# Performance work log

Hardware: AMD Instinct MI355X
Metric: run time of the kernel (lower is better)

Reference implementation:

```python
import jax, jax.numpy as jnp
import numpy as np

N_NODES = 100000
N_EDGES = 1600000
IN_CH = 64
HID = 64
OUT_CH = 16


def setup_inputs() -> dict:
    key = jax.random.key(0)
    ks = jax.random.split(key, 8)
    x = jax.random.normal(ks[0], (N_NODES, IN_CH), dtype=jnp.float32)
    edge_index = jax.random.randint(ks[1], (2, N_EDGES), 0, N_NODES, dtype=jnp.int64)
    s = 1.0 / np.sqrt(IN_CH)
    W1l = jax.random.normal(ks[2], (HID, IN_CH), dtype=jnp.float32) * s
    W1r = jax.random.normal(ks[3], (HID, IN_CH), dtype=jnp.float32) * s
    b1 = jnp.zeros((HID,), dtype=jnp.float32)
    W2l = jax.random.normal(ks[4], (HID, HID), dtype=jnp.float32) * s
    W2r = jax.random.normal(ks[5], (HID, HID), dtype=jnp.float32) * s
    b2 = jnp.zeros((HID,), dtype=jnp.float32)
    Wlin = jax.random.normal(ks[6], (OUT_CH, HID), dtype=jnp.float32) * s
    blin = jnp.zeros((OUT_CH,), dtype=jnp.float32)
    return {"x": x, "edge_index": edge_index, "W1l": W1l, "b1": b1, "W1r": W1r,
            "W2l": W2l, "b2": b2, "W2r": W2r, "Wlin": Wlin, "blin": blin}


def _sage_conv(x, src, dst, Wl, b, Wr):
    # PyG SAGEConv with mean aggregation:
    # out = lin_l(mean_{j in N(i)} x_j) + lin_r(x_i); bias lives in lin_l.
    msgs = x[src]                                              # [E, F] gather
    summed = jax.ops.segment_sum(msgs, dst, num_segments=N_NODES)  # [N, F]
    cnt = jax.ops.segment_sum(jnp.ones((src.shape[0],), x.dtype), dst,
                              num_segments=N_NODES)            # [N]
    agg = summed / jnp.maximum(cnt, 1.0)[:, None]              # mean, deg-0 safe
    return agg @ Wl.T + b + x @ Wr.T


def reference(x, edge_index, W1l, b1, W1r, W2l, b2, W2r, Wlin, blin):
    src, dst = edge_index[0], edge_index[1]
    h = jax.nn.relu(_sage_conv(x, src, dst, W1l, b1, W1r))
    h = jax.nn.relu(_sage_conv(h, src, dst, W2l, b2, W2r))
    return h @ Wlin.T + blin
```

## Files before the change

kernel.cpp:

```cpp
#include <hip/hip_runtime.h>

#define NN 100000
#define NE 1600000

#define BSHIFT 9
#define BWIDTH 512
#define NBUCK 196
#define SLOTS 12288
#define CHUNK 2048
#define B1_BLOCKS ((NE + CHUNK - 1) / CHUNK)
#define GEMM_BLOCKS ((NN + 63) / 64)

typedef float    v2f __attribute__((ext_vector_type(2)));
typedef unsigned v2u __attribute__((ext_vector_type(2)));
typedef short    bf16x8 __attribute__((ext_vector_type(8)));
typedef float    f32x4  __attribute__((ext_vector_type(4)));

__device__ __forceinline__ float u2f(unsigned u) {
    union { unsigned u; float f; } v; v.u = u; return v.f;
}
__device__ __forceinline__ unsigned f2u(float f) {
    union { float f; unsigned u; } v; v.f = f; return v.u;
}
__device__ __forceinline__ unsigned f2bf(float f) {
    unsigned u = f2u(f);
    return (u + 0x7FFFu + ((u >> 16) & 1u)) >> 16;
}
__device__ __forceinline__ v2f unpk(unsigned x) {
    v2u w; w[0] = x << 16; w[1] = x & 0xFFFF0000u;
    union { v2u u; v2f f; } c; c.u = w; return c.f;
}

__global__ void detect_mode_kernel(const int* ei32, int* flag, int* bcnt) {
    __shared__ int any_nonzero;
    if (threadIdx.x == 0) any_nonzero = 0;
    if (threadIdx.x < NBUCK) bcnt[threadIdx.x] = 0;
    __syncthreads();
    int idx = 1 + 2 * threadIdx.x;
    if (ei32[idx] != 0) atomicOr(&any_nonzero, 1);
    __syncthreads();
    if (threadIdx.x == 0) flag[0] = (any_nonzero == 0) ? 1 : 0;
}

__device__ __forceinline__ void load_edge(const void* ei, int is64, int e,
                                          int& s, int& d) {
    if (is64) {
        const long long* p = (const long long*)ei;
        s = (int)p[e];
        d = (int)p[NE + e];
    } else {
        const int* p = (const int*)ei;
        s = p[e];
        d = p[NE + e];
    }
}

template<int BF16IN>
__device__ __forceinline__ void gemm_mfma_body(
    char* smem, const void* __restrict__ featv,
    const float* __restrict__ Wl, const float* __restrict__ Wr,
    const float* __restrict__ bias,
    unsigned* __restrict__ outt, unsigned* __restrict__ outr,
    int tile, int t)
{
    unsigned short* Als = (unsigned short*)smem;
    unsigned short* Bls = (unsigned short*)(smem + 9216);
    const int lane = t & 63, w = t >> 6;
    const int m0 = tile * 64;
    const float*    featf = (const float*)featv;
    const unsigned* featu = (const unsigned*)featv;

    #pragma unroll
    for (int rep = 0; rep < 2; ++rep) {
        int task = t + 256 * rep;
        int row = task >> 3, s = task & 7;
        int gn = m0 + row;
        uint4 u;
        if (BF16IN) {
            u = (gn < NN) ? *(const uint4*)(featu + (size_t)gn * 32 + 4 * s)
                          : make_uint4(0u, 0u, 0u, 0u);
        } else {
            if (gn < NN) {
                float4 v0 = *(const float4*)(featf + (size_t)gn * 64 + 8 * s);
                float4 v1 = *(const float4*)(featf + (size_t)gn * 64 + 8 * s + 4);
                u.x = f2bf(v0.x) | (f2bf(v0.y) << 16);
                u.y = f2bf(v0.z) | (f2bf(v0.w) << 16);
                u.z = f2bf(v1.x) | (f2bf(v1.y) << 16);
                u.w = f2bf(v1.z) | (f2bf(v1.w) << 16);
            } else u = make_uint4(0u, 0u, 0u, 0u);
        }
        *(uint4*)(Als + row * 72 + 8 * s) = u;
    }
    #pragma unroll
    for (int rep = 0; rep < 4; ++rep) {
        int task = t + 256 * rep;
        int c = task >> 3, s = task & 7;
        const float* Wsrc = (c < 64) ? (Wl + (size_t)c * 64)
                                     : (Wr + (size_t)(c - 64) * 64);
        float4 v0 = *(const float4*)(Wsrc + 8 * s);
        float4 v1 = *(const float4*)(Wsrc + 8 * s + 4);
        uint4 u;
        u.x = f2bf(v0.x) | (f2bf(v0.y) << 16);
        u.y = f2bf(v0.z) | (f2bf(v0.w) << 16);
        u.z = f2bf(v1.x) | (f2bf(v1.y) << 16);
        u.w = f2bf(v1.z) | (f2bf(v1.w) << 16);
        *(uint4*)(Bls + c * 72 + 8 * s) = u;
    }
    __syncthreads();

    const int r = lane & 15, g = lane >> 4;
    const int cw0 = 32 * w;

    bf16x8 bf[2][2];
    #pragma unroll
    for (int ct = 0; ct < 2; ++ct)
        #pragma unroll
        for (int ks = 0; ks < 2; ++ks) {
            int c = cw0 + 16 * ct + r;
            bf[ct][ks] = *(const bf16x8*)(Bls + c * 72 + (ks * 4 + g) * 8);
        }

    f32x4 acc[4][2];
    #pragma unroll
    for (int nt = 0; nt < 4; ++nt)
        #pragma unroll
        for (int ct = 0; ct < 2; ++ct)
            acc[nt][ct] = (f32x4){0.f, 0.f, 0.f, 0.f};

    #pragma unroll
    for (int nt = 0; nt < 4; ++nt) {
        bf16x8 af[2];
        #pragma unroll
        for (int ks = 0; ks < 2; ++ks) {
            int rr = nt * 16 + r;
            af[ks] = *(const bf16x8*)(Als + rr * 72 + (ks * 4 + g) * 8);
        }
        #pragma unroll
        for (int ct = 0; ct < 2; ++ct)
            #pragma unroll
            for (int ks = 0; ks < 2; ++ks)
                acc[nt][ct] = __builtin_amdgcn_mfma_f32_16x16x32_bf16(
                    af[ks], bf[ct][ks], acc[nt][ct], 0, 0, 0);
    }

    unsigned short* Tb = (unsigned short*)outt;
    unsigned short* Rb = (unsigned short*)outr;
    #pragma unroll
    for (int ct = 0; ct < 2; ++ct) {
        int c = cw0 + 16 * ct + r;
        float badd = (c >= 64) ? bias[c - 64] : 0.f;
        unsigned short* dst = (c < 64) ? (Tb + c) : (Rb + (c - 64));
        #pragma unroll
        for (int nt = 0; nt < 4; ++nt)
            #pragma unroll
            for (int i = 0; i < 4; ++i) {
                int row = m0 + nt * 16 + g * 4 + i;
                if (row < NN)
                    dst[(size_t)row * 64] = (unsigned short)f2bf(acc[nt][ct][i] + badd);
            }
    }
}

__global__ __launch_bounds__(256) void b1_gemm1_kernel(
    const void* ei, const int* flag,
    int* __restrict__ bcnt, int2* __restrict__ bpairs,
    const float* __restrict__ x,
    const float* __restrict__ W1l, const float* __restrict__ W1r,
    const float* __restrict__ b1,
    unsigned* __restrict__ T, unsigned* __restrict__ R)
{
    __shared__ __align__(16) char smem[27648];
    const int t = threadIdx.x;

    if (blockIdx.x >= B1_BLOCKS) {
        if (blockIdx.x == B1_BLOCKS && t < 32) T[(size_t)NN * 32 + t] = 0u;
        gemm_mfma_body<0>(smem, x, W1l, W1r, b1, T, R, blockIdx.x - B1_BLOCKS, t);
        return;
    }

    int2* stage = (int2*)smem;
    unsigned short* sbuck = (unsigned short*)(smem + 16384);
    int* hist  = (int*)(smem + 20480);
    int* scanb = (int*)(smem + 21264);
    int* gbase = (int*)(smem + 22048);
    int* lofs  = (int*)(smem + 22832);
    int* sc    = (int*)(smem + 23616);

    const int is64 = *flag;
    const int e0 = blockIdx.x * CHUNK;
    const int nE = min(CHUNK, NE - e0);

    for (int i = t; i < NBUCK; i += 256) { hist[i] = 0; lofs[i] = 0; }
    __syncthreads();

    int sr[8], dr[8];
    #pragma unroll
    for (int rr = 0; rr < 8; ++rr) {
        int e = e0 + t + 256 * rr;
        if (e < NE) load_edge(ei, is64, e, sr[rr], dr[rr]);
        else dr[rr] = -1;
    }
    #pragma unroll
    for (int rr = 0; rr < 8; ++rr)
        if (dr[rr] >= 0) atomicAdd(&hist[dr[rr] >> BSHIFT], 1);
    __syncthreads();

    int v = (t < NBUCK) ? hist[t] : 0;
    sc[t] = v;
    __syncthreads();
    for (int off = 1; off < 256; off <<= 1) {
        int u = (t >= off) ? sc[t - off] : 0;
        __syncthreads();
        sc[t] += u;
        __syncthreads();
    }
    if (t < NBUCK) {
        scanb[t] = sc[t] - v;
        gbase[t] = atomicAdd(&bcnt[t], v);
    }
    __syncthreads();

    #pragma unroll
    for (int rr = 0; rr < 8; ++rr) {
        if (dr[rr] >= 0) {
            int b = dr[rr] >> BSHIFT;
            int p = scanb[b] + atomicAdd(&lofs[b], 1);
            stage[p] = make_int2(sr[rr], dr[rr]);
            sbuck[p] = (unsigned short)b;
        }
    }
    __syncthreads();

    for (int i = t; i < nE; i += 256) {
        int b = sbuck[i];
        int off = gbase[b] + (i - scanb[b]);
        if (off < SLOTS) bpairs[(size_t)b * SLOTS + off] = stage[i];
    }
}

__global__ __launch_bounds__(512) void bucket_to_csr_kernel(
    const int* __restrict__ bcnt, const int2* __restrict__ bpairs,
    int* __restrict__ rowptr, int* __restrict__ colb)
{
    __shared__ int ldeg[512], lptr[512], lcnt[512], sc[512];
    const int t = threadIdx.x, b = blockIdx.x;

    int v = (t < NBUCK) ? bcnt[t] : 0;
    sc[t] = v;
    __syncthreads();
    for (int off = 1; off < 512; off <<= 1) {
        int u = (t >= off) ? sc[t - off] : 0;
        __syncthreads();
        sc[t] += u;
        __syncthreads();
    }
    const int base = (b == 0) ? 0 : sc[b - 1];
    if (b == 0 && t == 0) rowptr[NN] = NE;
    __syncthreads();

    ldeg[t] = 0; lcnt[t] = 0;
    __syncthreads();

    const int n0 = b << BSHIFT;
    const int cnt = min(bcnt[b], SLOTS);
    const int2* src = bpairs + (size_t)b * SLOTS;
    for (int i = t; i < cnt; i += 512)
        atomicAdd(&ldeg[src[i].y - n0], 1);
    __syncthreads();

    int a = ldeg[t];
    sc[t] = a;
    __syncthreads();
    for (int off = 1; off < 512; off <<= 1) {
        int u = (t >= off) ? sc[t - off] : 0;
        __syncthreads();
        sc[t] += u;
        __syncthreads();
    }
    lptr[t] = sc[t] - a;
    __syncthreads();

    int gn = n0 + t;
    if (gn < NN) rowptr[gn] = base + lptr[t];

    for (int i = t; i < cnt; i += 512) {
        int2 p = src[i];
        int li = p.y - n0;
        int pos = lptr[li] + atomicAdd(&lcnt[li], 1);
        colb[base + pos] = p.x << 7;
    }
}

__global__ __launch_bounds__(256) void gemm2_kernel(
    const unsigned* __restrict__ feat,
    const float* __restrict__ Wl, const float* __restrict__ Wr,
    const float* __restrict__ bias,
    unsigned* __restrict__ outt, unsigned* __restrict__ outr)
{
    __shared__ __align__(16) char smem[27648];
    gemm_mfma_body<1>(smem, feat, Wl, Wr, bias, outt, outr, blockIdx.x, threadIdx.x);
}

__global__ void aggregate_relu_kernel(const int* __restrict__ rowptr,
                                      const int* __restrict__ colb,
                                      const unsigned* __restrict__ tt,
                                      unsigned* rh) {
    const int wv   = (blockIdx.x * blockDim.x + threadIdx.x) >> 6;
    const int lane = threadIdx.x & 63;
    const int half = lane >> 5;
    const int slot = (lane >> 3) & 3;
    const int c8   = lane & 7;
    const int node = 2 * wv + half;
    if (node >= NN) return;

    const int beg = rowptr[node], end = rowptr[node + 1];
    const int deg = end - beg;
    int niter = (deg + 3) >> 2;
    niter = max(niter, __shfl_xor(niter, 32));

    const char* tb = (const char*)tt;
    const int zoff = NN * 128;
    v2f a0 = {0.f, 0.f}, a1 = {0.f, 0.f}, a2 = {0.f, 0.f}, a3 = {0.f, 0.f};
    v2f b0 = {0.f, 0.f}, b1 = {0.f, 0.f}, b2 = {0.f, 0.f}, b3 = {0.f, 0.f};

    int jj = beg + slot;
    int it = 0;
    for (; it + 4 <= niter; it += 4, jj += 16) {
        int jc0 = min(jj,      end - 1);
        int jc1 = min(jj + 4,  end - 1);
        int jc2 = min(jj + 8,  end - 1);
        int jc3 = min(jj + 12, end - 1);
        int o0 = colb[jc0];
        int o1 = colb[jc1];
        int o2 = colb[jc2];
        int o3 = colb[jc3];
        o0 = (jj      < end) ? o0 : zoff;
        o1 = (jj + 4  < end) ? o1 : zoff;
        o2 = (jj + 8  < end) ? o2 : zoff;
        o3 = (jj + 12 < end) ? o3 : zoff;
        uint4 u0 = *(const uint4*)(tb + (size_t)(unsigned)o0 + 16 * c8);
        uint4 u1 = *(const uint4*)(tb + (size_t)(unsigned)o1 + 16 * c8);
        uint4 u2 = *(const uint4*)(tb + (size_t)(unsigned)o2 + 16 * c8);
        uint4 u3 = *(const uint4*)(tb + (size_t)(unsigned)o3 + 16 * c8);
        a0 += unpk(u0.x); a1 += unpk(u0.y); a2 += unpk(u0.z); a3 += unpk(u0.w);
        b0 += unpk(u1.x); b1 += unpk(u1.y); b2 += unpk(u1.z); b3 += unpk(u1.w);
        a0 += unpk(u2.x); a1 += unpk(u2.y); a2 += unpk(u2.z); a3 += unpk(u2.w);
        b0 += unpk(u3.x); b1 += unpk(u3.y); b2 += unpk(u3.z); b3 += unpk(u3.w);
    }
    for (; it < niter; ++it, jj += 4) {
        int jc0 = min(jj, end - 1);
        int o0 = colb[jc0];
        o0 = (jj < end) ? o0 : zoff;
        uint4 u0 = *(const uint4*)(tb + (size_t)(unsigned)o0 + 16 * c8);
        a0 += unpk(u0.x); a1 += unpk(u0.y); a2 += unpk(u0.z); a3 += unpk(u0.w);
    }
    a0 += b0; a1 += b1; a2 += b2; a3 += b3;

    a0[0] += __shfl_xor(a0[0], 8);  a0[1] += __shfl_xor(a0[1], 8);
    a1[0] += __shfl_xor(a1[0], 8);  a1[1] += __shfl_xor(a1[1], 8);
    a2[0] += __shfl_xor(a2[0], 8);  a2[1] += __shfl_xor(a2[1], 8);
    a3[0] += __shfl_xor(a3[0], 8);  a3[1] += __shfl_xor(a3[1], 8);
    a0[0] += __shfl_xor(a0[0], 16); a0[1] += __shfl_xor(a0[1], 16);
    a1[0] += __shfl_xor(a1[0], 16); a1[1] += __shfl_xor(a1[1], 16);
    a2[0] += __shfl_xor(a2[0], 16); a2[1] += __shfl_xor(a2[1], 16);
    a3[0] += __shfl_xor(a3[0], 16); a3[1] += __shfl_xor(a3[1], 16);

    if (slot == 0) {
        float inv = 1.0f / fmaxf((float)deg, 1.0f);
        unsigned* p = rh + (size_t)node * 32 + 4 * c8;
        uint4 rr = *(const uint4*)p;
        v2f q0 = unpk(rr.x), q1 = unpk(rr.y), q2 = unpk(rr.z), q3 = unpk(rr.w);
        float h0 = fmaxf(fmaf(a0[0], inv, q0[0]), 0.0f);
        float h1 = fmaxf(fmaf(a0[1], inv, q0[1]), 0.0f);
        float h2 = fmaxf(fmaf(a1[0], inv, q1[0]), 0.0f);
        float h3 = fmaxf(fmaf(a1[1], inv, q1[1]), 0.0f);
        float h4 = fmaxf(fmaf(a2[0], inv, q2[0]), 0.0f);
        float h5 = fmaxf(fmaf(a2[1], inv, q2[1]), 0.0f);
        float h6 = fmaxf(fmaf(a3[0], inv, q3[0]), 0.0f);
        float h7 = fmaxf(fmaf(a3[1], inv, q3[1]), 0.0f);
        uint4 wv4;
        wv4.x = f2bf(h0) | (f2bf(h1) << 16);
        wv4.y = f2bf(h2) | (f2bf(h3) << 16);
        wv4.z = f2bf(h4) | (f2bf(h5) << 16);
        wv4.w = f2bf(h6) | (f2bf(h7) << 16);
        *(uint4*)p = wv4;
    }
}

__global__ __launch_bounds__(256) void head_kernel(
    const unsigned* __restrict__ hu,
    const float* __restrict__ Wlin,
    const float* __restrict__ blin,
    float* __restrict__ out)
{
    __shared__ float As[64][132];
    __shared__ float Bs[64][18];
    const int t = threadIdx.x;

    {
        int c = t & 15, j = t >> 4;
        float4 v = *(const float4*)(Wlin + (size_t)c * 64 + 4 * j);
        Bs[4 * j + 0][c] = v.x; Bs[4 * j + 1][c] = v.y;
        Bs[4 * j + 2][c] = v.z; Bs[4 * j + 3][c] = v.w;
    }
    const int m0 = blockIdx.x * 128;
    {
        int kq = t & 7;
        int nb = t >> 3;
        for (int rep = 0; rep < 4; ++rep) {
            int n = nb + 32 * rep;
            int gn = m0 + n;
            uint4 u = (gn < NN) ? *(const uint4*)(hu + (size_t)gn * 32 + 4 * kq)
                                : make_uint4(0u, 0u, 0u, 0u);
            int kk = 8 * kq;
            As[kk + 0][n] = u2f(u.x << 16); As[kk + 1][n] = u2f(u.x & 0xFFFF0000u);
            As[kk + 2][n] = u2f(u.y << 16); As[kk + 3][n] = u2f(u.y & 0xFFFF0000u);
            As[kk + 4][n] = u2f(u.z << 16); As[kk + 5][n] = u2f(u.z & 0xFFFF0000u);
            As[kk + 6][n] = u2f(u.w << 16); As[kk + 7][n] = u2f(u.w & 0xFFFF0000u);
        }
    }
    __syncthreads();

    const int tn = t & 31;
    const int tc = t >> 5;
    const int c0 = 2 * tc;
    float acc[4][2];
    #pragma unroll
    for (int i = 0; i < 4; ++i) { acc[i][0] = blin[c0]; acc[i][1] = blin[c0 + 1]; }

    #pragma unroll 16
    for (int k = 0; k < 64; ++k) {
        float4 a = *(const float4*)&As[k][4 * tn];
        float b0 = Bs[k][c0], b1 = Bs[k][c0 + 1];
        float av[4] = {a.x, a.y, a.z, a.w};
        #pragma unroll
        for (int i = 0; i < 4; ++i) {
            acc[i][0] = fmaf(av[i], b0, acc[i][0]);
            acc[i][1] = fmaf(av[i], b1, acc[i][1]);
        }
    }
    #pragma unroll
    for (int i = 0; i < 4; ++i) {
        int gn = m0 + 4 * tn + i;
        if (gn < NN)
            *(float2*)(out + (size_t)gn * 16 + c0) = make_float2(acc[i][0], acc[i][1]);
    }
}

extern "C" void kernel_launch(void* const* d_in, const int* in_sizes, int n_in,
                              void* d_out, int out_size, void* d_ws, size_t ws_size,
                              hipStream_t stream) {
    const float* x    = (const float*)d_in[0];
    const void*  ei   = d_in[1];
    const float* W1l  = (const float*)d_in[2];
    const float* b1   = (const float*)d_in[3];
    const float* W1r  = (const float*)d_in[4];
    const float* W2l  = (const float*)d_in[5];
    const float* b2   = (const float*)d_in[6];
    const float* W2r  = (const float*)d_in[7];
    const float* Wlin = (const float*)d_in[8];
    const float* blin = (const float*)d_in[9];
    float* out = (float*)d_out;

    char* w = (char*)d_ws;
    int*      flag   = (int*)w;
    int*      bcnt   = (int*)(w + (size_t)4 * 1024);
    int*      rowptr = (int*)(w + (size_t)1024 * 1024);
    int*      colb   = (int*)(w + (size_t)2 * 1024 * 1024);
    int2*     bpairs = (int2*)(w + (size_t)10 * 1024 * 1024);
    unsigned* T      = (unsigned*)(w + (size_t)30 * 1024 * 1024);
    unsigned* R      = (unsigned*)(w + (size_t)43 * 1024 * 1024);

    detect_mode_kernel<<<1, 256, 0, stream>>>((const int*)ei, flag, bcnt);

    b1_gemm1_kernel<<<B1_BLOCKS + GEMM_BLOCKS, 256, 0, stream>>>(
        ei, flag, bcnt, bpairs, x, W1l, W1r, b1, T, R);

    bucket_to_csr_kernel<<<NBUCK, 512, 0, stream>>>(bcnt, bpairs, rowptr, colb);

    const int aggWaves  = (NN + 1) / 2;
    const int aggBlocks = (aggWaves * 64 + 255) / 256;
    const int headBlocks = (NN + 127) / 128;

    aggregate_relu_kernel<<<aggBlocks, 256, 0, stream>>>(rowptr, colb, T, R);

    gemm2_kernel<<<GEMM_BLOCKS, 256, 0, stream>>>(R, W2l, W2r, b2, T, R);
    aggregate_relu_kernel<<<aggBlocks, 256, 0, stream>>>(rowptr, colb, T, R);

    head_kernel<<<headBlocks, 256, 0, stream>>>(R, Wlin, blin, out);
}
```

Measured before the change: 153.6 us.

## Pack edge pairs into one int, wave-level scans, stage CSR columns in LDS

Bucketed edge pairs are stored as a single packed int (source shifted left plus local destination) instead of an int2, which halves the intermediate bucket traffic between the bucketing and CSR-build kernels. The shared-memory Hillis-Steele block scans are replaced with wave-shuffle scans plus a small cross-wave fixup, removing many barriers. The bucketing chunk per block grows to 4096 edges. The aggregation kernel now loads each block's 8-node column range into LDS before gathering, with a global-memory fallback when the range exceeds 1024 entries, at the cost of an extra barrier and LDS use.

```diff
diff --git a/kernel.cpp b/kernel.cpp
--- a/kernel.cpp
+++ b/kernel.cpp
@@ -7,9 +7,10 @@
 #define BWIDTH 512
 #define NBUCK 196
 #define SLOTS 12288
-#define CHUNK 2048
+#define CHUNK 4096
 #define B1_BLOCKS ((NE + CHUNK - 1) / CHUNK)
 #define GEMM_BLOCKS ((NN + 63) / 64)
+#define AGG_CAP 1024
 
 typedef float    v2f __attribute__((ext_vector_type(2)));
 typedef unsigned v2u __attribute__((ext_vector_type(2)));
@@ -29,6 +30,14 @@
 __device__ __forceinline__ v2f unpk(unsigned x) {
     v2u w; w[0] = x << 16; w[1] = x & 0xFFFF0000u;
     union { v2u u; v2f f; } c; c.u = w; return c.f;
+}
+__device__ __forceinline__ int wave_incl_scan(int v, int lane) {
+    #pragma unroll
+    for (int off = 1; off < 64; off <<= 1) {
+        int u = __shfl_up(v, off);
+        if (lane >= off) v += u;
+    }
+    return v;
 }
 
 __global__ void detect_mode_kernel(const int* ei32, int* flag, int* bcnt) {
@@ -163,7 +172,7 @@
 
 __global__ __launch_bounds__(256) void b1_gemm1_kernel(
     const void* ei, const int* flag,
-    int* __restrict__ bcnt, int2* __restrict__ bpairs,
+    int* __restrict__ bcnt, int* __restrict__ bpk,
     const float* __restrict__ x,
     const float* __restrict__ W1l, const float* __restrict__ W1r,
     const float* __restrict__ b1,
@@ -178,55 +187,55 @@
         return;
     }
 
-    int2* stage = (int2*)smem;
-    unsigned short* sbuck = (unsigned short*)(smem + 16384);
+    int* stage = (int*)smem;
+    unsigned char* sbuck = (unsigned char*)(smem + 16384);
     int* hist  = (int*)(smem + 20480);
     int* scanb = (int*)(smem + 21264);
     int* gbase = (int*)(smem + 22048);
     int* lofs  = (int*)(smem + 22832);
-    int* sc    = (int*)(smem + 23616);
+    int* wsum  = (int*)(smem + 23616);
 
     const int is64 = *flag;
     const int e0 = blockIdx.x * CHUNK;
     const int nE = min(CHUNK, NE - e0);
+    const int lane = t & 63, wvi = t >> 6;
 
     for (int i = t; i < NBUCK; i += 256) { hist[i] = 0; lofs[i] = 0; }
     __syncthreads();
 
-    int sr[8], dr[8];
-    #pragma unroll
-    for (int rr = 0; rr < 8; ++rr) {
+    int sr[16], dr[16];
+    #pragma unroll
+    for (int rr = 0; rr < 16; ++rr) {
         int e = e0 + t + 256 * rr;
         if (e < NE) load_edge(ei, is64, e, sr[rr], dr[rr]);
         else dr[rr] = -1;
     }
     #pragma unroll
-    for (int rr = 0; rr < 8; ++rr)
+    for (int rr = 0; rr < 16; ++rr)
         if (dr[rr] >= 0) atomicAdd(&hist[dr[rr] >> BSHIFT], 1);
     __syncthreads();
 
     int v = (t < NBUCK) ? hist[t] : 0;
-    sc[t] = v;
-    __syncthreads();
-    for (int off = 1; off < 256; off <<= 1) {
-        int u = (t >= off) ? sc[t - off] : 0;
-        __syncthreads();
-        sc[t] += u;
-        __syncthreads();
-    }
+    int s = wave_incl_scan(v, lane);
+    if (lane == 63) wsum[wvi] = s;
+    __syncthreads();
+    int add = 0;
+    #pragma unroll
+    for (int k = 0; k < 3; ++k) if (wvi > k) add += wsum[k];
+    s += add;
     if (t < NBUCK) {
-        scanb[t] = sc[t] - v;
+        scanb[t] = s - v;
         gbase[t] = atomicAdd(&bcnt[t], v);
     }
     __syncthreads();
 
     #pragma unroll
-    for (int rr = 0; rr < 8; ++rr) {
+    for (int rr = 0; rr < 16; ++rr) {
         if (dr[rr] >= 0) {
             int b = dr[rr] >> BSHIFT;
             int p = scanb[b] + atomicAdd(&lofs[b], 1);
-            stage[p] = make_int2(sr[rr], dr[rr]);
-            sbuck[p] = (unsigned short)b;
+            stage[p] = (sr[rr] << BSHIFT) | (dr[rr] & (BWIDTH - 1));
+            sbuck[p] = (unsigned char)b;
         }
     }
     __syncthreads();
@@ -234,26 +243,28 @@
     for (int i = t; i < nE; i += 256) {
         int b = sbuck[i];
         int off = gbase[b] + (i - scanb[b]);
-        if (off < SLOTS) bpairs[(size_t)b * SLOTS + off] = stage[i];
+        if (off < SLOTS) bpk[(size_t)b * SLOTS + off] = stage[i];
     }
 }
 
 __global__ __launch_bounds__(512) void bucket_to_csr_kernel(
-    const int* __restrict__ bcnt, const int2* __restrict__ bpairs,
+    const int* __restrict__ bcnt, const int* __restrict__ bpk,
     int* __restrict__ rowptr, int* __restrict__ colb)
 {
-    __shared__ int ldeg[512], lptr[512], lcnt[512], sc[512];
+    __shared__ int ldeg[512], lptr[512], lcnt[512], sc[512], wsum[8];
     const int t = threadIdx.x, b = blockIdx.x;
+    const int lane = t & 63, wvi = t >> 6;
 
     int v = (t < NBUCK) ? bcnt[t] : 0;
-    sc[t] = v;
-    __syncthreads();
-    for (int off = 1; off < 512; off <<= 1) {
-        int u = (t >= off) ? sc[t - off] : 0;
-        __syncthreads();
-        sc[t] += u;
-        __syncthreads();
-    }
+    int s = wave_incl_scan(v, lane);
+    if (lane == 63) wsum[wvi] = s;
+    __syncthreads();
+    int add = 0;
+    #pragma unroll
+    for (int k = 0; k < 7; ++k) if (wvi > k) add += wsum[k];
+    s += add;
+    sc[t] = s;
+    __syncthreads();
     const int base = (b == 0) ? 0 : sc[b - 1];
     if (b == 0 && t == 0) rowptr[NN] = NE;
     __syncthreads();
@@ -263,31 +274,30 @@
 
     const int n0 = b << BSHIFT;
     const int cnt = min(bcnt[b], SLOTS);
-    const int2* src = bpairs + (size_t)b * SLOTS;
+    const int* src = bpk + (size_t)b * SLOTS;
     for (int i = t; i < cnt; i += 512)
-        atomicAdd(&ldeg[src[i].y - n0], 1);
+        atomicAdd(&ldeg[src[i] & (BWIDTH - 1)], 1);
     __syncthreads();
 
     int a = ldeg[t];
-    sc[t] = a;
-    __syncthreads();
-    for (int off = 1; off < 512; off <<= 1) {
-        int u = (t >= off) ? sc[t - off] : 0;
-        __syncthreads();
-        sc[t] += u;
-        __syncthreads();
-    }
-    lptr[t] = sc[t] - a;
+    int s2 = wave_incl_scan(a, lane);
+    if (lane == 63) wsum[wvi] = s2;
+    __syncthreads();
+    int add2 = 0;
+    #pragma unroll
+    for (int k = 0; k < 7; ++k) if (wvi > k) add2 += wsum[k];
+    s2 += add2;
+    lptr[t] = s2 - a;
     __syncthreads();
 
     int gn = n0 + t;
     if (gn < NN) rowptr[gn] = base + lptr[t];
 
     for (int i = t; i < cnt; i += 512) {
-        int2 p = src[i];
-        int li = p.y - n0;
+        int p = src[i];
+        int li = p & (BWIDTH - 1);
         int pos = lptr[li] + atomicAdd(&lcnt[li], 1);
-        colb[base + pos] = p.x << 7;
+        colb[base + pos] = (p >> BSHIFT) << 7;
     }
 }
 
@@ -301,18 +311,47 @@
     gemm_mfma_body<1>(smem, feat, Wl, Wr, bias, outt, outr, blockIdx.x, threadIdx.x);
 }
 
+#define AGG_STEP(O0, O1, O2, O3)                                              \
+    {                                                                         \
+        int o0 = O0, o1 = O1, o2 = O2, o3 = O3;                               \
+        o0 = (jj      < end) ? o0 : zoff;                                     \
+        o1 = (jj + 4  < end) ? o1 : zoff;                                     \
+        o2 = (jj + 8  < end) ? o2 : zoff;                                     \
+        o3 = (jj + 12 < end) ? o3 : zoff;                                     \
+        uint4 u0 = *(const uint4*)(tb + (size_t)(unsigned)o0 + 16 * c8);      \
+        uint4 u1 = *(const uint4*)(tb + (size_t)(unsigned)o1 + 16 * c8);      \
+        uint4 u2 = *(const uint4*)(tb + (size_t)(unsigned)o2 + 16 * c8);      \
+        uint4 u3 = *(const uint4*)(tb + (size_t)(unsigned)o3 + 16 * c8);      \
+        a0 += unpk(u0.x); a1 += unpk(u0.y); a2 += unpk(u0.z); a3 += unpk(u0.w);\
+        b0 += unpk(u1.x); b1 += unpk(u1.y); b2 += unpk(u1.z); b3 += unpk(u1.w);\
+        a0 += unpk(u2.x); a1 += unpk(u2.y); a2 += unpk(u2.z); a3 += unpk(u2.w);\
+        b0 += unpk(u3.x); b1 += unpk(u3.y); b2 += unpk(u3.z); b3 += unpk(u3.w);\
+    }
+
 __global__ void aggregate_relu_kernel(const int* __restrict__ rowptr,
                                       const int* __restrict__ colb,
                                       const unsigned* __restrict__ tt,
                                       unsigned* rh) {
-    const int wv   = (blockIdx.x * blockDim.x + threadIdx.x) >> 6;
-    const int lane = threadIdx.x & 63;
+    __shared__ int lcol[AGG_CAP];
+    const int t = threadIdx.x;
+    const int n0 = blockIdx.x * 8;
+    const int lane = t & 63;
+    const int w = t >> 6;
     const int half = lane >> 5;
     const int slot = (lane >> 3) & 3;
     const int c8   = lane & 7;
-    const int node = 2 * wv + half;
+    const int node = n0 + 2 * w + half;
+
+    const int cbeg  = rowptr[n0];
+    const int cendB = rowptr[min(n0 + 8, NN)];
+    const int total = cendB - cbeg;
+    const bool fast = (total <= AGG_CAP);
+    if (fast) {
+        for (int i = t; i < total; i += 256) lcol[i] = colb[cbeg + i];
+    }
+    __syncthreads();
+
     if (node >= NN) return;
-
     const int beg = rowptr[node], end = rowptr[node + 1];
     const int deg = end - beg;
     int niter = (deg + 3) >> 2;
@@ -325,34 +364,36 @@
 
     int jj = beg + slot;
     int it = 0;
-    for (; it + 4 <= niter; it += 4, jj += 16) {
-        int jc0 = min(jj,      end - 1);
-        int jc1 = min(jj + 4,  end - 1);
-        int jc2 = min(jj + 8,  end - 1);
-        int jc3 = min(jj + 12, end - 1);
-        int o0 = colb[jc0];
-        int o1 = colb[jc1];
-        int o2 = colb[jc2];
-        int o3 = colb[jc3];
-        o0 = (jj      < end) ? o0 : zoff;
-        o1 = (jj + 4  < end) ? o1 : zoff;
-        o2 = (jj + 8  < end) ? o2 : zoff;
-        o3 = (jj + 12 < end) ? o3 : zoff;
-        uint4 u0 = *(const uint4*)(tb + (size_t)(unsigned)o0 + 16 * c8);
-        uint4 u1 = *(const uint4*)(tb + (size_t)(unsigned)o1 + 16 * c8);
-        uint4 u2 = *(const uint4*)(tb + (size_t)(unsigned)o2 + 16 * c8);
-        uint4 u3 = *(const uint4*)(tb + (size_t)(unsigned)o3 + 16 * c8);
-        a0 += unpk(u0.x); a1 += unpk(u0.y); a2 += unpk(u0.z); a3 += unpk(u0.w);
-        b0 += unpk(u1.x); b1 += unpk(u1.y); b2 += unpk(u1.z); b3 += unpk(u1.w);
-        a0 += unpk(u2.x); a1 += unpk(u2.y); a2 += unpk(u2.z); a3 += unpk(u2.w);
-        b0 += unpk(u3.x); b1 += unpk(u3.y); b2 += unpk(u3.z); b3 += unpk(u3.w);
-    }
-    for (; it < niter; ++it, jj += 4) {
-        int jc0 = min(jj, end - 1);
-        int o0 = colb[jc0];
-        o0 = (jj < end) ? o0 : zoff;
-        uint4 u0 = *(const uint4*)(tb + (size_t)(unsigned)o0 + 16 * c8);
-        a0 += unpk(u0.x); a1 += unpk(u0.y); a2 += unpk(u0.z); a3 += unpk(u0.w);
+    if (fast) {
+        for (; it + 4 <= niter; it += 4, jj += 16) {
+            int jc0 = min(jj,      end - 1) - cbeg;
+            int jc1 = min(jj + 4,  end - 1) - cbeg;
+            int jc2 = min(jj + 8,  end - 1) - cbeg;
+            int jc3 = min(jj + 12, end - 1) - cbeg;
+            AGG_STEP(lcol[jc0], lcol[jc1], lcol[jc2], lcol[jc3])
+        }
+        for (; it < niter; ++it, jj += 4) {
+            int jc0 = min(jj, end - 1) - cbeg;
+            int o0 = lcol[jc0];
+            o0 = (jj < end) ? o0 : zoff;
+            uint4 u0 = *(const uint4*)(tb + (size_t)(unsigned)o0 + 16 * c8);
+            a0 += unpk(u0.x); a1 += unpk(u0.y); a2 += unpk(u0.z); a3 += unpk(u0.w);
+        }
+    } else {
+        for (; it + 4 <= niter; it += 4, jj += 16) {
+            int jc0 = min(jj,      end - 1);
+            int jc1 = min(jj + 4,  end - 1);
+            int jc2 = min(jj + 8,  end - 1);
+            int jc3 = min(jj + 12, end - 1);
+            AGG_STEP(colb[jc0], colb[jc1], colb[jc2], colb[jc3])
+        }
+        for (; it < niter; ++it, jj += 4) {
+            int jc0 = min(jj, end - 1);
+            int o0 = colb[jc0];
+            o0 = (jj < end) ? o0 : zoff;
+            uint4 u0 = *(const uint4*)(tb + (size_t)(unsigned)o0 + 16 * c8);
+            a0 += unpk(u0.x); a1 += unpk(u0.y); a2 += unpk(u0.z); a3 += unpk(u0.w);
+        }
     }
     a0 += b0; a1 += b1; a2 += b2; a3 += b3;
 
@@ -467,19 +508,18 @@
     int*      bcnt   = (int*)(w + (size_t)4 * 1024);
     int*      rowptr = (int*)(w + (size_t)1024 * 1024);
     int*      colb   = (int*)(w + (size_t)2 * 1024 * 1024);
-    int2*     bpairs = (int2*)(w + (size_t)10 * 1024 * 1024);
+    int*      bpk    = (int*)(w + (size_t)10 * 1024 * 1024);
     unsigned* T      = (unsigned*)(w + (size_t)30 * 1024 * 1024);
     unsigned* R      = (unsigned*)(w + (size_t)43 * 1024 * 1024);
 
     detect_mode_kernel<<<1, 256, 0, stream>>>((const int*)ei, flag, bcnt);
 
     b1_gemm1_kernel<<<B1_BLOCKS + GEMM_BLOCKS, 256, 0, stream>>>(
-        ei, flag, bcnt, bpairs, x, W1l, W1r, b1, T, R);
-
-    bucket_to_csr_kernel<<<NBUCK, 512, 0, stream>>>(bcnt, bpairs, rowptr, colb);
-
-    const int aggWaves  = (NN + 1) / 2;
-    const int aggBlocks = (aggWaves * 64 + 255) / 256;
+        ei, flag, bcnt, bpk, x, W1l, W1r, b1, T, R);
+
+    bucket_to_csr_kernel<<<NBUCK, 512, 0, stream>>>(bcnt, bpk, rowptr, colb);
+
+    const int aggBlocks = (NN + 7) / 8;
     const int headBlocks = (NN + 127) / 128;
 
     aggregate_relu_kernel<<<aggBlocks, 256, 0, stream>>>(rowptr, colb, T, R);
```

Result: faster. 144.5 us (-5.9%).
